# Kernel optimization log

Hardware: AMD Instinct MI355X
Metric: run time of the kernel (lower is better)

## Reference

```python
import jax, jax.numpy as jnp
import numpy as np

REDUCTION_SIZE = 2


def setup_inputs() -> dict:
    key = jax.random.key(0)
    k1, k2 = jax.random.split(key)
    T, E, K, D = 32768, 256, 8, 8  # tokens, experts, top-k, devices
    topk_tensor = jax.random.normal(k1, (1, 1, T, E), dtype=jnp.float32)
    # one-hot expert -> device mapping (contiguous blocks of E//D experts per device)
    dev_of_expert = jnp.arange(E, dtype=jnp.int32) // (E // D)
    expert_mapping = jax.nn.one_hot(dev_of_expert, D, dtype=jnp.int32)[None, None]  # [1,1,E,D]
    expert_metadata = jax.random.randint(k2, (1, 1, T, K), 0, E, dtype=jnp.int32)[None][0]
    return {
        "topk_tensor": topk_tensor,
        "expert_mapping": expert_mapping,
        "expert_metadata": expert_metadata,
    }


def reference(topk_tensor, expert_mapping, expert_metadata):
    r = REDUCTION_SIZE
    topk = topk_tensor[0, 0]          # [T, E] scores over all experts
    mapping = expert_mapping[0, 0]    # [E, D] one-hot expert->device
    meta = expert_metadata[0, 0]      # [T, K] selected expert indices
    T, E = topk.shape
    D = mapping.shape[-1]

    dev_of_expert = jnp.argmax(mapping, axis=-1)            # [E]
    tok_dev = dev_of_expert[meta]                           # [T, K] device of each selected expert

    # token -> device dispatch mask, reduced over groups of `r` tokens
    rows = jnp.arange(T, dtype=jnp.int32)[:, None]
    mask = jnp.zeros((T, D), dtype=jnp.int32).at[rows, tok_dev].set(1)  # [T, D]
    reduced_mask = mask.reshape(T // r, r, D).max(axis=1)               # [T//r, D]

    # selection mask over experts (scatter, avoids [T,K,E] one-hot blowup)
    sel = jnp.zeros((T, E), dtype=topk.dtype).at[rows, meta].set(1.0)   # [T, E]
    gated = topk * sel                                                  # zero non-selected scores

    # remap expert columns into device-local slots
    perm = jnp.argsort(dev_of_expert, stable=True)                      # experts grouped by device
    remapped = gated[:, perm].reshape(T, D, E // D).transpose(1, 0, 2)  # [D, T, E//D]
    return remapped, reduced_mask
```

## Files before the change

### kernel.cpp

```cpp
#include <hip/hip_runtime.h>

#define T_TOK 32768
#define E_EXP 256
#define K_SEL 8
#define D_DEV 8
#define SLOTS (E_EXP / D_DEV)
#define TOK_PER_BLK 32

typedef float floatx4 __attribute__((ext_vector_type(4)));

__global__ __launch_bounds__(256) void zero_remap_kernel(
    float* __restrict__ out_remap) {
  const size_t i = (size_t)blockIdx.x * 256 + threadIdx.x;
  const floatx4 z4 = {0.f, 0.f, 0.f, 0.f};
  floatx4* o = (floatx4*)out_remap;
#pragma unroll
  for (int r = 0; r < 4; ++r)
    o[i + (size_t)r * (2048u * 256u)] = z4;
}

__global__ __launch_bounds__(256) void scatter_kernel(
    const float* __restrict__ topk, const int* __restrict__ mapping,
    const int* __restrict__ meta, float* __restrict__ out_remap,
    float* __restrict__ out_mask) {
  __shared__ int sdev[E_EXP];
  __shared__ int spos[E_EXP];
  __shared__ int scnt[4 * D_DEV];

  const int tid  = threadIdx.x;
  const int w    = tid >> 6;
  const int lane = tid & 63;
  const int tbase = blockIdx.x * TOK_PER_BLK;
  const int tl = tid >> 3;

  const int e = meta[(size_t)tbase * K_SEL + tid];
  const float sc = topk[(size_t)(tbase + tl) * E_EXP + e];

  const int4 m0 = ((const int4*)mapping)[tid * 2];
  const int4 m1 = ((const int4*)mapping)[tid * 2 + 1];

  {
    int vals[8] = {m0.x, m0.y, m0.z, m0.w, m1.x, m1.y, m1.z, m1.w};
    int best = vals[0], dev = 0;
#pragma unroll
    for (int d = 1; d < 8; ++d)
      if (vals[d] > best) { best = vals[d]; dev = d; }
    sdev[tid] = dev;

    unsigned long long myball = 0ull;
#pragma unroll
    for (int d = 0; d < 8; ++d) {
      unsigned long long b = __ballot(dev == d);
      if (d == dev) myball = b;
      if (lane == d) scnt[w * 8 + d] = __popcll(b);
    }
    const unsigned long long lt = (lane == 0) ? 0ull : (~0ull >> (64 - lane));
    const int lower = __popcll(myball & lt);
    __syncthreads();
    int base = 0;
    for (int d = 0; d < dev; ++d)
      base += scnt[0 * 8 + d] + scnt[1 * 8 + d] + scnt[2 * 8 + d] +
              scnt[3 * 8 + d];
    for (int w2 = 0; w2 < w; ++w2) base += scnt[w2 * 8 + dev];
    spos[tid] = base + lower;
  }
  __syncthreads();

  const int pos = spos[e];
  const int dv  = sdev[e];

  {
    unsigned long long bsel = 0ull;
#pragma unroll
    for (int d = 0; d < D_DEV; ++d) {
      unsigned long long b = __ballot(dv == d);
      if ((lane & 7) == d) bsel = b;
    }
    if (lane < 32) {
      const float fm =
          ((bsel >> (16 * (lane >> 3))) & 0xFFFFull) ? 1.0f : 0.0f;
      const int rowi = (tbase >> 1) + (w << 2) + (lane >> 3);
      out_mask[(size_t)rowi * D_DEV + (lane & 7)] = fm;
    }
  }

  float* dst = out_remap + (size_t)(pos >> 5) * T_TOK * SLOTS +
               (size_t)(tbase + tl) * SLOTS + (pos & 31);
  __builtin_nontemporal_store(sc, dst);
}

extern "C" void kernel_launch(void* const* d_in, const int* in_sizes, int n_in,
                              void* d_out, int out_size, void* d_ws, size_t ws_size,
                              hipStream_t stream) {
  const float* topk    = (const float*)d_in[0];
  const int*   mapping = (const int*)d_in[1];
  const int*   meta    = (const int*)d_in[2];

  float* out_remap = (float*)d_out;
  float* out_mask  = out_remap + (size_t)D_DEV * T_TOK * SLOTS;

  zero_remap_kernel<<<2048, 256, 0, stream>>>(out_remap);
  scatter_kernel<<<T_TOK / TOK_PER_BLK, 256, 0, stream>>>(
      topk, mapping, meta, out_remap, out_mask);
}
```

Measured before the change: 90.55 us.

## Fuse zeroing and scatter into one kernel via shared-memory dense row tiles

Replaces the separate zero-fill kernel and scattered per-element stores with one kernel that builds 16-token dense output rows in LDS (zero, scatter selected scores, then write out with coalesced vector stores). This removes the second full pass over the large output and the partial-cacheline scattered writes. Each block now handles 64 tokens in 4 iterations with prefetch of the next scores, at the cost of extra barriers and only a fraction of threads doing the gather.

```diff
diff --git a/kernel.cpp b/kernel.cpp
--- a/kernel.cpp
+++ b/kernel.cpp
@@ -5,24 +5,20 @@
 #define K_SEL 8
 #define D_DEV 8
 #define SLOTS (E_EXP / D_DEV)
-#define TOK_PER_BLK 32
+#define NBLK  512
+#define BTHR  1024
+#define TOK_PER_BLK 64
+#define TOK_PER_IT  16
+#define NIT   4
+#define ROWP  264
 
 typedef float floatx4 __attribute__((ext_vector_type(4)));
 
-__global__ __launch_bounds__(256) void zero_remap_kernel(
-    float* __restrict__ out_remap) {
-  const size_t i = (size_t)blockIdx.x * 256 + threadIdx.x;
-  const floatx4 z4 = {0.f, 0.f, 0.f, 0.f};
-  floatx4* o = (floatx4*)out_remap;
-#pragma unroll
-  for (int r = 0; r < 4; ++r)
-    o[i + (size_t)r * (2048u * 256u)] = z4;
-}
-
-__global__ __launch_bounds__(256) void scatter_kernel(
+__global__ __launch_bounds__(BTHR, 8) void moe_fused_kernel(
     const float* __restrict__ topk, const int* __restrict__ mapping,
     const int* __restrict__ meta, float* __restrict__ out_remap,
     float* __restrict__ out_mask) {
+  __shared__ float tile[TOK_PER_IT * ROWP];
   __shared__ int sdev[E_EXP];
   __shared__ int spos[E_EXP];
   __shared__ int scnt[4 * D_DEV];
@@ -33,15 +29,21 @@
   const int tbase = blockIdx.x * TOK_PER_BLK;
   const int tl = tid >> 3;
 
-  const int e = meta[(size_t)tbase * K_SEL + tid];
-  const float sc = topk[(size_t)(tbase + tl) * E_EXP + e];
+  int e[NIT] = {0, 0, 0, 0};
+  float sc_cur = 0.0f;
+  if (tid < 128) {
+#pragma unroll
+    for (int i = 0; i < NIT; ++i)
+      e[i] = meta[(size_t)(tbase + i * TOK_PER_IT) * K_SEL + tid];
+    sc_cur = topk[(size_t)(tbase + tl) * E_EXP + e[0]];
+  }
 
-  const int4 m0 = ((const int4*)mapping)[tid * 2];
-  const int4 m1 = ((const int4*)mapping)[tid * 2 + 1];
-
-  {
+  int dev = 0, lower = 0;
+  if (tid < 256) {
+    const int4 m0 = ((const int4*)mapping)[tid * 2];
+    const int4 m1 = ((const int4*)mapping)[tid * 2 + 1];
     int vals[8] = {m0.x, m0.y, m0.z, m0.w, m1.x, m1.y, m1.z, m1.w};
-    int best = vals[0], dev = 0;
+    int best = vals[0];
 #pragma unroll
     for (int d = 1; d < 8; ++d)
       if (vals[d] > best) { best = vals[d]; dev = d; }
@@ -55,8 +57,10 @@
       if (lane == d) scnt[w * 8 + d] = __popcll(b);
     }
     const unsigned long long lt = (lane == 0) ? 0ull : (~0ull >> (64 - lane));
-    const int lower = __popcll(myball & lt);
-    __syncthreads();
+    lower = __popcll(myball & lt);
+  }
+  __syncthreads();
+  if (tid < 256) {
     int base = 0;
     for (int d = 0; d < dev; ++d)
       base += scnt[0 * 8 + d] + scnt[1 * 8 + d] + scnt[2 * 8 + d] +
@@ -66,27 +70,54 @@
   }
   __syncthreads();
 
-  const int pos = spos[e];
-  const int dv  = sdev[e];
+  const floatx4 z4 = {0.f, 0.f, 0.f, 0.f};
 
-  {
-    unsigned long long bsel = 0ull;
 #pragma unroll
-    for (int d = 0; d < D_DEV; ++d) {
-      unsigned long long b = __ballot(dv == d);
-      if ((lane & 7) == d) bsel = b;
+  for (int i = 0; i < NIT; ++i) {
+    float sc_next = 0.0f;
+    if (i + 1 < NIT && tid < 128)
+      sc_next =
+          topk[(size_t)(tbase + (i + 1) * TOK_PER_IT + tl) * E_EXP + e[i + 1]];
+
+    {
+      const int a = ((tid >> 3) & 15) * ROWP + (tid >> 7) * SLOTS +
+                    (tid & 7) * 4;
+      *(floatx4*)&tile[a] = z4;
     }
-    if (lane < 32) {
-      const float fm =
-          ((bsel >> (16 * (lane >> 3))) & 0xFFFFull) ? 1.0f : 0.0f;
-      const int rowi = (tbase >> 1) + (w << 2) + (lane >> 3);
-      out_mask[(size_t)rowi * D_DEV + (lane & 7)] = fm;
+    __syncthreads();
+
+    if (tid < 128) {
+      const int pos = spos[e[i]];
+      const int dv  = sdev[e[i]];
+      tile[tl * ROWP + pos] = sc_cur;
+
+      unsigned long long bsel = 0ull;
+#pragma unroll
+      for (int d = 0; d < D_DEV; ++d) {
+        unsigned long long b = __ballot(dv == d);
+        if ((lane & 7) == d) bsel = b;
+      }
+      if (lane < 32) {
+        const float fm =
+            ((bsel >> (16 * (lane >> 3))) & 0xFFFFull) ? 1.0f : 0.0f;
+        const int rowi =
+            ((tbase + i * TOK_PER_IT) >> 1) + (w << 2) + (lane >> 3);
+        out_mask[(size_t)rowi * D_DEV + (lane & 7)] = fm;
+      }
     }
+    __syncthreads();
+
+    {
+      const int t16    = (tid >> 3) & 15;
+      const int dchunk = tid >> 7;
+      const int j      = (tid & 7) * 4;
+      const floatx4 v = *(const floatx4*)&tile[t16 * ROWP + dchunk * SLOTS + j];
+      *(floatx4*)(out_remap + (size_t)dchunk * T_TOK * SLOTS +
+                  (size_t)(tbase + i * TOK_PER_IT + t16) * SLOTS + j) = v;
+    }
+    sc_cur = sc_next;
+    __syncthreads();
   }
-
-  float* dst = out_remap + (size_t)(pos >> 5) * T_TOK * SLOTS +
-               (size_t)(tbase + tl) * SLOTS + (pos & 31);
-  __builtin_nontemporal_store(sc, dst);
 }
 
 extern "C" void kernel_launch(void* const* d_in, const int* in_sizes, int n_in,
@@ -99,7 +130,6 @@
   float* out_remap = (float*)d_out;
   float* out_mask  = out_remap + (size_t)D_DEV * T_TOK * SLOTS;
 
-  zero_remap_kernel<<<2048, 256, 0, stream>>>(out_remap);
-  scatter_kernel<<<T_TOK / TOK_PER_BLK, 256, 0, stream>>>(
-      topk, mapping, meta, out_remap, out_mask);
+  moe_fused_kernel<<<NBLK, BTHR, 0, stream>>>(topk, mapping, meta, out_remap,
+                                              out_mask);
 }
```

After: 86.91 us. 4.0% less time.
